# Kernel tuning notes

Hardware: AMD Instinct MI355X
Metric: run time of the kernel (lower is better)

Reference implementation:

```python
import jax, jax.numpy as jnp
import numpy as np

L = 64       # num_steps
NHID = 256   # nhid
N = 64       # cache_N
TOPK = 8     # cache_k


def setup_inputs() -> dict:
    key = jax.random.key(0)
    k1, k2, k3 = jax.random.split(key, 3)
    query = jax.random.normal(k1, (1, L, 32, NHID), dtype=jnp.float32)
    keys = jax.random.normal(k2, (N, 32, L * NHID), dtype=jnp.float32)       # stacked key_i buffers
    values = jax.random.normal(k3, (N, L, 32, 4 * NHID), dtype=jnp.float32)  # stacked value_i buffers, (nlayers+1)*nhid=1024
    return {"query": query, "keys": keys, "values": values}


def reference(query, keys, values):
    # query: (query_len=1, L, bsz, nhid) -> transpose(1,2) -> (1, bsz, L, nhid)
    q = jnp.swapaxes(query, 1, 2)
    qlen, bsz = q.shape[0], q.shape[1]
    q = q.reshape(qlen, bsz, -1)                 # no_summary: (1, bsz, dk)
    keys_t = jnp.swapaxes(keys, 0, 1)            # (bsz, N, dk)
    _vals = jnp.einsum('klbh->bklh', values)     # (bsz, N, L, h); computed in original, unused in max_pooling branch
    # max_pooling branch
    q2 = q.reshape(-1, L, NHID)                  # (bsz, L, nhid)
    pk = keys_t.reshape(-1, N, L, NHID)          # (bsz, N, L, nhid)
    att = jnp.einsum('bih,bnjh->bijn', q2, pk)   # (bsz, L, L, N)
    att = att.reshape(-1, L * L, 1, N).max(axis=1)  # (bsz, 1, N) max-pool over all step pairs
    att = att.reshape(-1, 1, N)
    _, topk_idx = jax.lax.top_k(att, TOPK)       # (bsz, 1, topk)
    topk_idx = jnp.squeeze(topk_idx, axis=1).T   # (topk, bsz)
    return att, topk_idx
```

## Files before the change

kernel.cpp:

```cpp
#include <hip/hip_runtime.h>
#include <hip/hip_bf16.h>
#include <math.h>

namespace {

constexpr int L   = 64;
constexpr int NH  = 256;
constexpr int NC  = 64;
constexpr int BSZ = 32;

typedef float f32x16 __attribute__((ext_vector_type(16)));
typedef short bf16x8 __attribute__((ext_vector_type(8)));

__device__ inline void split8(const float4 x0, const float4 x1,
                              bf16x8& hi, bf16x8& lo) {
  float f[8];
  *(float4*)(f)     = x0;
  *(float4*)(f + 4) = x1;
#pragma unroll
  for (int q = 0; q < 8; ++q) {
    const __hip_bfloat16 h = __float2bfloat16(f[q]);
    unsigned short hu;
    __builtin_memcpy(&hu, &h, 2);
    const float hf = __builtin_bit_cast(float, (unsigned)hu << 16);
    const __hip_bfloat16 l = __float2bfloat16(f[q] - hf);
    unsigned short lu;
    __builtin_memcpy(&lu, &l, 2);
    hi[q] = (short)hu;
    lo[q] = (short)lu;
  }
}

__device__ inline void gl16(const void* g, void* l) {
  __builtin_amdgcn_global_load_lds(
      (const __attribute__((address_space(1))) unsigned*)(g),
      (__attribute__((address_space(3))) unsigned*)(l), 16, 0, 0);
}

__global__ __launch_bounds__(256) void qsplit_kernel(
    const float* __restrict__ query, char* __restrict__ ws) {
  const int b   = blockIdx.x;
  const int tid = threadIdx.x;
  char* wb = ws + (size_t)b * 65536;
#pragma unroll
  for (int rr = 0; rr < 8; ++rr) {
    const int s  = tid + rr * 256;
    const int it = s >> 10;
    const int kc = (s >> 6) & 15;
    const int sl = s & 63;
    const int row = it * 32 + (sl & 31);
    const int kof = kc * 16 + (sl >> 5) * 8;
    const float* src = query + ((size_t)row * BSZ + b) * NH + kof;
    bf16x8 hi, lo;
    split8(*(const float4*)src, *(const float4*)(src + 4), hi, lo);
    *(bf16x8*)(wb + (size_t)s * 16)         = hi;
    *(bf16x8*)(wb + 32768 + (size_t)s * 16) = lo;
  }
}

__global__ __launch_bounds__(512, 4) void attmax_mfma(
    const float* __restrict__ keys,
    const char* __restrict__ ws,
    float* __restrict__ out)
{
  __shared__ __align__(16) char qlds[64 * 1024];
  __shared__ float wm[8];
  const short* Qhi = (const short*)qlds;
  const short* Qlo = (const short*)(qlds + 32768);

  const unsigned X = blockIdx.x;
  const int b  = X & 31;
  const int ng = X >> 5;

  const int tid  = threadIdx.x;
  const int w    = tid >> 6;
  const int lane = tid & 63;
  const int n    = ng * 4 + (w >> 1);
  const int jt   = w & 1;

  {
    const char* src = ws + (size_t)b * 65536;
#pragma unroll
    for (int q = 0; q < 8; ++q) {
      const int off = (q * 8 + w) * 1024;
      gl16(src + off + lane * 16, qlds + off);
    }
  }
  __syncthreads();

  const float* kp = keys + ((size_t)n * BSZ + b) * (size_t)(L * NH)
                  + (size_t)(jt * 32 + (lane & 31)) * NH + (lane >> 5) * 8;

  f32x16 acc[2];
#pragma unroll
  for (int it = 0; it < 2; ++it)
#pragma unroll
    for (int e = 0; e < 16; ++e) acc[it][e] = 0.f;

  float4 bufA[2], bufB[2];

#define LOAD_K(buf, kc)                                  \
  do {                                                   \
    const float* p0 = kp + (kc) * 16;                    \
    (buf)[0] = *(const float4*)(p0);                     \
    (buf)[1] = *(const float4*)(p0 + 4);                 \
  } while (0)

#define COMPUTE(buf, kc)                                                      \
  do {                                                                        \
    bf16x8 bh, bl;                                                            \
    split8((buf)[0], (buf)[1], bh, bl);                                       \
    _Pragma("unroll")                                                         \
    for (int it = 0; it < 2; ++it) {                                          \
      const int slot = ((it * 16 + (kc)) * 64 + lane) * 8;                    \
      const bf16x8 ah = *(const bf16x8*)&Qhi[slot];                           \
      const bf16x8 al = *(const bf16x8*)&Qlo[slot];                           \
      acc[it] = __builtin_amdgcn_mfma_f32_32x32x16_bf16(al, bh, acc[it], 0, 0, 0); \
      acc[it] = __builtin_amdgcn_mfma_f32_32x32x16_bf16(ah, bl, acc[it], 0, 0, 0); \
      acc[it] = __builtin_amdgcn_mfma_f32_32x32x16_bf16(ah, bh, acc[it], 0, 0, 0); \
    }                                                                         \
  } while (0)

  LOAD_K(bufA, 0);
#pragma unroll
  for (int kc = 0; kc < 16; kc += 2) {
    if (kc + 1 < 16) LOAD_K(bufB, kc + 1);
    COMPUTE(bufA, kc);
    if (kc + 2 < 16) LOAD_K(bufA, kc + 2);
    COMPUTE(bufB, kc + 1);
  }
#undef LOAD_K
#undef COMPUTE

  float m = -INFINITY;
#pragma unroll
  for (int it = 0; it < 2; ++it)
#pragma unroll
    for (int e = 0; e < 16; ++e) m = fmaxf(m, acc[it][e]);
#pragma unroll
  for (int off = 1; off < 64; off <<= 1)
    m = fmaxf(m, __shfl_xor(m, off, 64));

  if (lane == 0) wm[w] = m;
  __syncthreads();
  if (lane == 0 && (w & 1) == 0)
    out[(size_t)b * NC + n] = fmaxf(wm[w], wm[w + 1]);
}

__global__ __launch_bounds__(64) void topk_kernel(float* __restrict__ out) {
  const int b = blockIdx.x;
  const int l = threadIdx.x;
  float v = out[b * NC + l];
#pragma unroll
  for (int k = 0; k < 8; ++k) {
    float bv = v;
    int bi = l;
#pragma unroll
    for (int off = 1; off < 64; off <<= 1) {
      const float ov = __shfl_xor(bv, off, 64);
      const int oi = __shfl_xor(bi, off, 64);
      if (ov > bv || (ov == bv && oi < bi)) { bv = ov; bi = oi; }
    }
    if (l == 0) out[BSZ * NC + k * BSZ + b] = (float)bi;
    if (l == bi) v = -INFINITY;
  }
}

}

extern "C" void kernel_launch(void* const* d_in, const int* in_sizes, int n_in,
                              void* d_out, int out_size, void* d_ws, size_t ws_size,
                              hipStream_t stream) {
  const float* query = (const float*)d_in[0];
  const float* keys  = (const float*)d_in[1];
  float* out = (float*)d_out;
  char*  ws  = (char*)d_ws;

  qsplit_kernel<<<dim3(BSZ), dim3(256), 0, stream>>>(query, ws);
  attmax_mfma<<<dim3(512), dim3(512), 0, stream>>>(keys, ws, out);
  topk_kernel<<<dim3(BSZ), dim3(64), 0, stream>>>(out);
}
```

Before: 40.30 us.

## Fuse top-k into attention kernel via last-block atomic and triple-buffer key loads

```diff
diff --git a/kernel.cpp b/kernel.cpp
--- a/kernel.cpp
+++ b/kernel.cpp
@@ -39,9 +39,10 @@
 
 __global__ __launch_bounds__(256) void qsplit_kernel(
     const float* __restrict__ query, char* __restrict__ ws) {
+  if (blockIdx.x == 0 && threadIdx.x == 0) *(unsigned*)ws = 0u;
   const int b   = blockIdx.x;
   const int tid = threadIdx.x;
-  char* wb = ws + (size_t)b * 65536;
+  char* wb = ws + 4096 + (size_t)b * 65536;
 #pragma unroll
   for (int rr = 0; rr < 8; ++rr) {
     const int s  = tid + rr * 256;
@@ -60,11 +61,12 @@
 
 __global__ __launch_bounds__(512, 4) void attmax_mfma(
     const float* __restrict__ keys,
-    const char* __restrict__ ws,
+    char* __restrict__ ws,
     float* __restrict__ out)
 {
   __shared__ __align__(16) char qlds[64 * 1024];
   __shared__ float wm[8];
+  __shared__ int lastFlag;
   const short* Qhi = (const short*)qlds;
   const short* Qlo = (const short*)(qlds + 32768);
 
@@ -79,7 +81,7 @@
   const int jt   = w & 1;
 
   {
-    const char* src = ws + (size_t)b * 65536;
+    const char* src = ws + 4096 + (size_t)b * 65536;
 #pragma unroll
     for (int q = 0; q < 8; ++q) {
       const int off = (q * 8 + w) * 1024;
@@ -97,19 +99,19 @@
 #pragma unroll
     for (int e = 0; e < 16; ++e) acc[it][e] = 0.f;
 
-  float4 bufA[2], bufB[2];
+  float4 K0[2], K1[2], K2[2];
 
-#define LOAD_K(buf, kc)                                  \
+#define LOAD_K(B, kc)                                    \
   do {                                                   \
     const float* p0 = kp + (kc) * 16;                    \
-    (buf)[0] = *(const float4*)(p0);                     \
-    (buf)[1] = *(const float4*)(p0 + 4);                 \
+    (B)[0] = *(const float4*)(p0);                       \
+    (B)[1] = *(const float4*)(p0 + 4);                   \
   } while (0)
 
-#define COMPUTE(buf, kc)                                                      \
+#define COMPUTE(B, kc)                                                        \
   do {                                                                        \
     bf16x8 bh, bl;                                                            \
-    split8((buf)[0], (buf)[1], bh, bl);                                       \
+    split8((B)[0], (B)[1], bh, bl);                                           \
     _Pragma("unroll")                                                         \
     for (int it = 0; it < 2; ++it) {                                          \
       const int slot = ((it * 16 + (kc)) * 64 + lane) * 8;                    \
@@ -121,16 +123,22 @@
     }                                                                         \
   } while (0)
 
-  LOAD_K(bufA, 0);
-#pragma unroll
-  for (int kc = 0; kc < 16; kc += 2) {
-    if (kc + 1 < 16) LOAD_K(bufB, kc + 1);
-    COMPUTE(bufA, kc);
-    if (kc + 2 < 16) LOAD_K(bufA, kc + 2);
-    COMPUTE(bufB, kc + 1);
-  }
+#define STEP(B, kc, kn)                                  \
+  do {                                                   \
+    COMPUTE(B, kc);                                      \
+    if ((kn) < 16) LOAD_K(B, kn);                        \
+  } while (0)
+
+  LOAD_K(K0, 0); LOAD_K(K1, 1); LOAD_K(K2, 2);
+  STEP(K0, 0, 3);   STEP(K1, 1, 4);   STEP(K2, 2, 5);
+  STEP(K0, 3, 6);   STEP(K1, 4, 7);   STEP(K2, 5, 8);
+  STEP(K0, 6, 9);   STEP(K1, 7, 10);  STEP(K2, 8, 11);
+  STEP(K0, 9, 12);  STEP(K1, 10, 13); STEP(K2, 11, 14);
+  STEP(K0, 12, 15); STEP(K1, 13, 16); STEP(K2, 14, 17);
+  STEP(K0, 15, 18);
 #undef LOAD_K
 #undef COMPUTE
+#undef STEP
 
   float m = -INFINITY;
 #pragma unroll
@@ -145,24 +153,30 @@
   __syncthreads();
   if (lane == 0 && (w & 1) == 0)
     out[(size_t)b * NC + n] = fmaxf(wm[w], wm[w + 1]);
-}
 
-__global__ __launch_bounds__(64) void topk_kernel(float* __restrict__ out) {
-  const int b = blockIdx.x;
-  const int l = threadIdx.x;
-  float v = out[b * NC + l];
-#pragma unroll
-  for (int k = 0; k < 8; ++k) {
-    float bv = v;
-    int bi = l;
-#pragma unroll
-    for (int off = 1; off < 64; off <<= 1) {
-      const float ov = __shfl_xor(bv, off, 64);
-      const int oi = __shfl_xor(bi, off, 64);
-      if (ov > bv || (ov == bv && oi < bi)) { bv = ov; bi = oi; }
+  __threadfence();
+  if (tid == 0) {
+    const unsigned t = atomicAdd((unsigned*)ws, 1u);
+    lastFlag = (t == gridDim.x - 1);
+  }
+  __syncthreads();
+  if (lastFlag) {
+    __threadfence();
+    if (tid < BSZ) {
+      const int bb = tid;
+      unsigned long long sel = 0ull;
+      for (int k = 0; k < 8; ++k) {
+        float best = -INFINITY;
+        int bi = 0;
+        for (int j = 0; j < 64; ++j) {
+          if ((sel >> j) & 1ull) continue;
+          const float v = out[bb * NC + j];
+          if (v > best) { best = v; bi = j; }
+        }
+        sel |= 1ull << bi;
+        out[BSZ * NC + k * BSZ + bb] = (float)bi;
+      }
     }
-    if (l == 0) out[BSZ * NC + k * BSZ + b] = (float)bi;
-    if (l == bi) v = -INFINITY;
   }
 }
 
@@ -178,5 +192,4 @@
 
   qsplit_kernel<<<dim3(BSZ), dim3(256), 0, stream>>>(query, ws);
   attmax_mfma<<<dim3(512), dim3(512), 0, stream>>>(keys, ws, out);
-  topk_kernel<<<dim3(BSZ), dim3(64), 0, stream>>>(out);
 }
```

Result: slower. 149.2 us (+270.2%).

## Switch to 16x16x32 MFMA tiles and spread query split over more blocks

Applied to the files above, without the earlier changes.

```diff
diff --git a/kernel.cpp b/kernel.cpp
--- a/kernel.cpp
+++ b/kernel.cpp
@@ -9,7 +9,7 @@
 constexpr int NC  = 64;
 constexpr int BSZ = 32;
 
-typedef float f32x16 __attribute__((ext_vector_type(16)));
+typedef float f32x4 __attribute__((ext_vector_type(4)));
 typedef short bf16x8 __attribute__((ext_vector_type(8)));
 
 __device__ inline void split8(const float4 x0, const float4 x1,
@@ -37,25 +37,23 @@
       (__attribute__((address_space(3))) unsigned*)(l), 16, 0, 0);
 }
 
+
 __global__ __launch_bounds__(256) void qsplit_kernel(
     const float* __restrict__ query, char* __restrict__ ws) {
-  const int b   = blockIdx.x;
-  const int tid = threadIdx.x;
+  const int X = blockIdx.x;
+  const int b = X >> 3;
+  const int s = (X & 7) * 256 + threadIdx.x;
+  const int it = s >> 9;
+  const int kc = (s >> 6) & 7;
+  const int l  = s & 63;
+  const int row = it * 16 + (l & 15);
+  const int col = kc * 32 + ((l >> 4) & 3) * 4;
+  const float* src = query + ((size_t)row * BSZ + b) * NH + col;
+  bf16x8 hi, lo;
+  split8(*(const float4*)src, *(const float4*)(src + 16), hi, lo);
   char* wb = ws + (size_t)b * 65536;
-#pragma unroll
-  for (int rr = 0; rr < 8; ++rr) {
-    const int s  = tid + rr * 256;
-    const int it = s >> 10;
-    const int kc = (s >> 6) & 15;
-    const int sl = s & 63;
-    const int row = it * 32 + (sl & 31);
-    const int kof = kc * 16 + (sl >> 5) * 8;
-    const float* src = query + ((size_t)row * BSZ + b) * NH + kof;
-    bf16x8 hi, lo;
-    split8(*(const float4*)src, *(const float4*)(src + 4), hi, lo);
-    *(bf16x8*)(wb + (size_t)s * 16)         = hi;
-    *(bf16x8*)(wb + 32768 + (size_t)s * 16) = lo;
-  }
+  *(bf16x8*)(wb + (size_t)s * 16)         = hi;
+  *(bf16x8*)(wb + 32768 + (size_t)s * 16) = lo;
 }
 
 __global__ __launch_bounds__(512, 4) void attmax_mfma(
@@ -75,8 +73,8 @@
   const int tid  = threadIdx.x;
   const int w    = tid >> 6;
   const int lane = tid & 63;
-  const int n    = ng * 4 + (w >> 1);
-  const int jt   = w & 1;
+  const int n     = ng * 4 + (w >> 1);
+  const int jhalf = w & 1;
 
   {
     const char* src = ws + (size_t)b * 65536;
@@ -88,55 +86,71 @@
   }
   __syncthreads();
 
-  const float* kp = keys + ((size_t)n * BSZ + b) * (size_t)(L * NH)
-                  + (size_t)(jt * 32 + (lane & 31)) * NH + (lane >> 5) * 8;
+  const float* kb = keys + ((size_t)n * BSZ + b) * (size_t)(L * NH)
+                  + (size_t)jhalf * 32 * NH;
+  const int rl = lane & 15;
+  const int cq = ((lane >> 4) & 3) * 4;
+  const float* kp0 = kb + (size_t)rl * NH + cq;
+  const float* kp1 = kb + (size_t)(16 + rl) * NH + cq;
 
-  f32x16 acc[2];
+  f32x4 acc[4][2];
 #pragma unroll
-  for (int it = 0; it < 2; ++it)
+  for (int it = 0; it < 4; ++it)
 #pragma unroll
-    for (int e = 0; e < 16; ++e) acc[it][e] = 0.f;
+    for (int jt = 0; jt < 2; ++jt)
+#pragma unroll
+      for (int e = 0; e < 4; ++e) acc[it][jt][e] = 0.f;
 
-  float4 bufA[2], bufB[2];
+  float4 K0[4], K1[4];
 
-#define LOAD_K(buf, kc)                                  \
+#define LOADC(B, kc)                                     \
   do {                                                   \
-    const float* p0 = kp + (kc) * 16;                    \
-    (buf)[0] = *(const float4*)(p0);                     \
-    (buf)[1] = *(const float4*)(p0 + 4);                 \
+    const float* p = kp0 + (kc) * 32;                    \
+    (B)[0] = *(const float4*)(p);                        \
+    (B)[1] = *(const float4*)(p + 16);                   \
+    const float* q = kp1 + (kc) * 32;                    \
+    (B)[2] = *(const float4*)(q);                        \
+    (B)[3] = *(const float4*)(q + 16);                   \
   } while (0)
 
-#define COMPUTE(buf, kc)                                                      \
+#define COMPC(B, kc)                                                          \
   do {                                                                        \
-    bf16x8 bh, bl;                                                            \
-    split8((buf)[0], (buf)[1], bh, bl);                                       \
+    bf16x8 bh0, bl0, bh1, bl1;                                                \
+    split8((B)[0], (B)[1], bh0, bl0);                                         \
+    split8((B)[2], (B)[3], bh1, bl1);                                         \
     _Pragma("unroll")                                                         \
-    for (int it = 0; it < 2; ++it) {                                          \
-      const int slot = ((it * 16 + (kc)) * 64 + lane) * 8;                    \
+    for (int it = 0; it < 4; ++it) {                                          \
+      const int slot = ((it * 8 + (kc)) * 64 + lane) * 8;                     \
       const bf16x8 ah = *(const bf16x8*)&Qhi[slot];                           \
       const bf16x8 al = *(const bf16x8*)&Qlo[slot];                           \
-      acc[it] = __builtin_amdgcn_mfma_f32_32x32x16_bf16(al, bh, acc[it], 0, 0, 0); \
-      acc[it] = __builtin_amdgcn_mfma_f32_32x32x16_bf16(ah, bl, acc[it], 0, 0, 0); \
-      acc[it] = __builtin_amdgcn_mfma_f32_32x32x16_bf16(ah, bh, acc[it], 0, 0, 0); \
+      acc[it][0] = __builtin_amdgcn_mfma_f32_16x16x32_bf16(al, bh0, acc[it][0], 0, 0, 0); \
+      acc[it][0] = __builtin_amdgcn_mfma_f32_16x16x32_bf16(ah, bl0, acc[it][0], 0, 0, 0); \
+      acc[it][0] = __builtin_amdgcn_mfma_f32_16x16x32_bf16(ah, bh0, acc[it][0], 0, 0, 0); \
+      acc[it][1] = __builtin_amdgcn_mfma_f32_16x16x32_bf16(al, bh1, acc[it][1], 0, 0, 0); \
+      acc[it][1] = __builtin_amdgcn_mfma_f32_16x16x32_bf16(ah, bl1, acc[it][1], 0, 0, 0); \
+      acc[it][1] = __builtin_amdgcn_mfma_f32_16x16x32_bf16(ah, bh1, acc[it][1], 0, 0, 0); \
     }                                                                         \
   } while (0)
 
-  LOAD_K(bufA, 0);
-#pragma unroll
-  for (int kc = 0; kc < 16; kc += 2) {
-    if (kc + 1 < 16) LOAD_K(bufB, kc + 1);
-    COMPUTE(bufA, kc);
-    if (kc + 2 < 16) LOAD_K(bufA, kc + 2);
-    COMPUTE(bufB, kc + 1);
-  }
-#undef LOAD_K
-#undef COMPUTE
+  LOADC(K0, 0); LOADC(K1, 1);
+  COMPC(K0, 0); LOADC(K0, 2);
+  COMPC(K1, 1); LOADC(K1, 3);
+  COMPC(K0, 2); LOADC(K0, 4);
+  COMPC(K1, 3); LOADC(K1, 5);
+  COMPC(K0, 4); LOADC(K0, 6);
+  COMPC(K1, 5); LOADC(K1, 7);
+  COMPC(K0, 6);
+  COMPC(K1, 7);
+#undef LOADC
+#undef COMPC
 
   float m = -INFINITY;
 #pragma unroll
-  for (int it = 0; it < 2; ++it)
+  for (int it = 0; it < 4; ++it)
 #pragma unroll
-    for (int e = 0; e < 16; ++e) m = fmaxf(m, acc[it][e]);
+    for (int jt = 0; jt < 2; ++jt)
+#pragma unroll
+      for (int e = 0; e < 4; ++e) m = fmaxf(m, acc[it][jt][e]);
 #pragma unroll
   for (int off = 1; off < 64; off <<= 1)
     m = fmaxf(m, __shfl_xor(m, off, 64));
@@ -176,7 +190,7 @@
   float* out = (float*)d_out;
   char*  ws  = (char*)d_ws;
 
-  qsplit_kernel<<<dim3(BSZ), dim3(256), 0, stream>>>(query, ws);
+  qsplit_kernel<<<dim3(256), dim3(256), 0, stream>>>(query, ws);
   attmax_mfma<<<dim3(512), dim3(512), 0, stream>>>(keys, ws, out);
   topk_kernel<<<dim3(BSZ), dim3(64), 0, stream>>>(out);
 }
```

Measured after the change: 40.82 us. About the same (+1.3%).
